# Kernel optimization log

Hardware: AMD Instinct MI355X
Metric: run time of the kernel (lower is better)

## Reference

```python
import jax, jax.numpy as jnp
import numpy as np

B, H, W, C = 4, 64, 64, 256
D = C // 8  # reduction_ratio = 8


def setup_inputs() -> dict:
    key = jax.random.key(0)
    ks = jax.random.split(key, 6)
    scale = 1.0 / np.sqrt(C)
    return {
        "x": jax.random.normal(ks[0], (B, H, W, C), dtype=jnp.float32),
        "Wf": jax.random.normal(ks[1], (C, D), dtype=jnp.float32) * scale,
        "Wg": jax.random.normal(ks[2], (C, D), dtype=jnp.float32) * scale,
        "Wh": jax.random.normal(ks[3], (C, D), dtype=jnp.float32) * scale,
        "Wv": jax.random.normal(ks[4], (D, C), dtype=jnp.float32) * (1.0 / np.sqrt(D)),
        "gamma": jax.random.normal(ks[5], (), dtype=jnp.float32),
    }


def reference(x, Wf, Wg, Wh, Wv, gamma):
    b, h, w, c = x.shape
    n = h * w
    xf = x.reshape(b, n, c)
    # 1x1 convs (no bias) == per-pixel matmuls over channels
    q = xf @ Wf  # [b, n, d]
    k = xf @ Wg  # [b, n, d]
    v = xf @ Wh  # [b, n, d]
    # beta[i, j] = k_i . q_j ; softmax over last (query) axis, unscaled
    beta = jax.nn.softmax(jnp.einsum('bnd,bmd->bnm', k, q), axis=-1)  # [b, n, n]
    o = jnp.einsum('bnm,bmd->bnd', beta, v)  # [b, n, d]
    o = o.reshape(b, h, w, -1) @ Wv  # output 1x1 conv -> [b, h, w, c]
    return gamma * o + x
```

## Files before the change

### kernel.cpp

```cpp
#include <hip/hip_runtime.h>
#include <hip/hip_bf16.h>
#include <stdint.h>


typedef __attribute__((ext_vector_type(8))) short bf16x8;
typedef __attribute__((ext_vector_type(4))) short bf16x4;
typedef __attribute__((ext_vector_type(4))) float f32x4;
typedef unsigned short ushort_t;

static __device__ __forceinline__ ushort_t f2bf(float f) {
    __hip_bfloat16 h = __float2bfloat16(f);
    return __builtin_bit_cast(ushort_t, h);
}
static __device__ __forceinline__ float bf2f(ushort_t u) {
    return __bfloat162float(__builtin_bit_cast(__hip_bfloat16, u));
}

static __device__ __forceinline__ f32x4 mfma16bf(bf16x4 a, bf16x4 b, f32x4 c) {
#if __has_builtin(__builtin_amdgcn_mfma_f32_16x16x16bf16_1k)
    return __builtin_amdgcn_mfma_f32_16x16x16bf16_1k(a, b, c, 0, 0, 0);
#else
    f32x4 d;
    asm("v_mfma_f32_16x16x16_bf16 %0, %1, %2, %3"
        : "=v"(d) : "v"(a), "v"(b), "v"(c));
    return d;
#endif
}

#define NROWS 16384
#define NTOK  4096
#define QKS   40
#define OPART (NROWS * 32)

__global__ __launch_bounds__(256) void qkv_kernel(
    const float* __restrict__ x,
    const float* __restrict__ Wf, const float* __restrict__ Wg,
    const float* __restrict__ Wh,
    ushort_t* __restrict__ qh,
    ushort_t* __restrict__ kh, ushort_t* __restrict__ kl,
    ushort_t* __restrict__ vT)
{
    __shared__ __align__(16) ushort_t xh[32 * QKS];
    __shared__ __align__(16) ushort_t xl[32 * QKS];

    const int tid  = threadIdx.x;
    const int wave = tid >> 6;
    const int lane = tid & 63;
    const int ln15 = lane & 15;
    const int quad = lane >> 4;
    const int row0 = blockIdx.x * 32;
    const int rg     = wave & 1;
    const int cgbase = wave >> 1;
    const int r  = tid >> 3;
    const int pp = (tid & 7) * 4;

    f32x4 acc[3];
    #pragma unroll
    for (int ci = 0; ci < 3; ++ci) acc[ci] = (f32x4){0.f, 0.f, 0.f, 0.f};

    float4 xa = *reinterpret_cast<const float4*>(&x[(row0 + r) * 256 + pp]);

    for (int k0 = 0; k0 < 256; k0 += 32) {
        bf16x8 bh[3], bl[3];
        #pragma unroll
        for (int ci = 0; ci < 3; ++ci) {
            int cg = cgbase + ci * 2;
            const float* Wsrc = (cg < 2) ? Wf : (cg < 4) ? Wg : Wh;
            int c = (cg & 1) * 16 + ln15;
            ushort_t hv8[8], lv8[8];
            #pragma unroll
            for (int j = 0; j < 8; ++j) {
                float w = Wsrc[(k0 + quad * 8 + j) * 32 + c];
                ushort_t hi = f2bf(w);
                hv8[j] = hi;
                lv8[j] = f2bf(w - bf2f(hi));
            }
            bh[ci] = *reinterpret_cast<bf16x8*>(hv8);
            bl[ci] = *reinterpret_cast<bf16x8*>(lv8);
        }
        float fv[4];
        *reinterpret_cast<float4*>(fv) = xa;
        ushort_t hv[4], lv[4];
        #pragma unroll
        for (int j = 0; j < 4; ++j) {
            hv[j] = f2bf(fv[j]);
            lv[j] = f2bf(fv[j] - bf2f(hv[j]));
        }
        __syncthreads();
        *reinterpret_cast<uint2*>(&xh[r * QKS + pp]) = *reinterpret_cast<uint2*>(hv);
        *reinterpret_cast<uint2*>(&xl[r * QKS + pp]) = *reinterpret_cast<uint2*>(lv);
        __syncthreads();
        if (k0 < 224)
            xa = *reinterpret_cast<const float4*>(&x[(row0 + r) * 256 + k0 + 32 + pp]);

        const bf16x8 ah = *reinterpret_cast<const bf16x8*>(
            &xh[(rg * 16 + ln15) * QKS + quad * 8]);
        const bf16x8 al = *reinterpret_cast<const bf16x8*>(
            &xl[(rg * 16 + ln15) * QKS + quad * 8]);
        #pragma unroll
        for (int ci = 0; ci < 3; ++ci) {
            acc[ci] = __builtin_amdgcn_mfma_f32_16x16x32_bf16(ah, bh[ci], acc[ci], 0, 0, 0);
            acc[ci] = __builtin_amdgcn_mfma_f32_16x16x32_bf16(al, bh[ci], acc[ci], 0, 0, 0);
            acc[ci] = __builtin_amdgcn_mfma_f32_16x16x32_bf16(ah, bl[ci], acc[ci], 0, 0, 0);
        }
    }

    #pragma unroll
    for (int ci = 0; ci < 3; ++ci) {
        int cg = cgbase + ci * 2;
        int cc = (cg & 1) * 16 + ln15;
        int rowb = row0 + rg * 16 + quad * 4;
        if (cg < 2) {
            #pragma unroll
            for (int rr = 0; rr < 4; ++rr)
                qh[(rowb + rr) * 32 + cc] = f2bf(acc[ci][rr]);
        } else if (cg < 4) {
            #pragma unroll
            for (int rr = 0; rr < 4; ++rr) {
                float val = acc[ci][rr];
                ushort_t hi = f2bf(val);
                kh[(rowb + rr) * 32 + cc] = hi;
                kl[(rowb + rr) * 32 + cc] = f2bf(val - bf2f(hi));
            }
        } else {
            int bb = row0 >> 12;
            int m  = (row0 & 4095) + rg * 16 + quad * 4;
            ushort4 h4;
            h4.x = f2bf(acc[ci][0]);
            h4.y = f2bf(acc[ci][1]);
            h4.z = f2bf(acc[ci][2]);
            h4.w = f2bf(acc[ci][3]);
            *reinterpret_cast<ushort4*>(&vT[bb * 131072 + cc * 4096 + m]) = h4;
        }
    }
}

__global__ __launch_bounds__(256, 4) void attn_kernel(
    const ushort_t* __restrict__ qhg,
    const ushort_t* __restrict__ khg, const ushort_t* __restrict__ klg,
    const ushort_t* __restrict__ vT,
    float* __restrict__ o_part, float* __restrict__ l_part)
{
    __shared__ float Ored[4][32][65];
    __shared__ float Lred[4][64];

    const int tid  = threadIdx.x;
    const int wave = tid >> 6;
    const int lane = tid & 63;
    const int ln15 = lane & 15;
    const int quad = lane >> 4;

    const int rowtile = blockIdx.x & 255;
    const int chunk   = blockIdx.x >> 8;
    const int b    = rowtile >> 6;
    const int n0   = (rowtile & 63) * 64;
    const int base = b * NTOK;
    const int bb   = b * 131072;

    bf16x8 khf[4], klf[4];
    #pragma unroll
    for (int t = 0; t < 4; ++t) {
        khf[t] = *reinterpret_cast<const bf16x8*>(
            &khg[(base + n0 + t * 16 + ln15) * 32 + quad * 8]);
        klf[t] = *reinterpret_cast<const bf16x8*>(
            &klg[(base + n0 + t * 16 + ln15) * 32 + quad * 8]);
    }

    f32x4 accO[2][4];
    #pragma unroll
    for (int s01 = 0; s01 < 2; ++s01)
        #pragma unroll
        for (int t = 0; t < 4; ++t)
            accO[s01][t] = (f32x4){0.f, 0.f, 0.f, 0.f};
    float lacc[4] = {0.f, 0.f, 0.f, 0.f};

    const int mbase = chunk * 1024 + wave * 16;
    const ushort_t* qp  = qhg + (size_t)(base + mbase + ln15) * 32 + quad * 8;
    const ushort_t* vp0 = vT + bb + ln15 * 4096 + mbase + quad * 4;
    const ushort_t* vp1 = vp0 + 16 * 4096;

    for (int it = 0; it < 16; ++it) {
        const bf16x8 qf  = *reinterpret_cast<const bf16x8*>(qp);
        const bf16x4 va0 = *reinterpret_cast<const bf16x4*>(vp0);
        const bf16x4 va1 = *reinterpret_cast<const bf16x4*>(vp1);
        qp  += 64 * 32;
        vp0 += 64;
        vp1 += 64;

        #pragma unroll
        for (int t = 0; t < 4; ++t) {
            f32x4 s = __builtin_amdgcn_mfma_f32_16x16x32_bf16(
                qf, khf[t], (f32x4){0.f, 0.f, 0.f, 0.f}, 0, 0, 0);
            s = __builtin_amdgcn_mfma_f32_16x16x32_bf16(qf, klf[t], s, 0, 0, 0);

            float p0 = __expf(s[0]);
            float p1 = __expf(s[1]);
            float p2 = __expf(s[2]);
            float p3 = __expf(s[3]);
            lacc[t] += (p0 + p1) + (p2 + p3);

            ushort_t pu[4];
            pu[0] = f2bf(p0);
            pu[1] = f2bf(p1);
            pu[2] = f2bf(p2);
            pu[3] = f2bf(p3);
            const bf16x4 pb = *reinterpret_cast<bf16x4*>(pu);

            accO[0][t] = mfma16bf(va0, pb, accO[0][t]);
            accO[1][t] = mfma16bf(va1, pb, accO[1][t]);
        }
    }

    #pragma unroll
    for (int s01 = 0; s01 < 2; ++s01)
        #pragma unroll
        for (int t = 0; t < 4; ++t)
            #pragma unroll
            for (int rr = 0; rr < 4; ++rr)
                Ored[wave][s01 * 16 + quad * 4 + rr][t * 16 + ln15] = accO[s01][t][rr];

    #pragma unroll
    for (int t = 0; t < 4; ++t) {
        float v = lacc[t];
        v += __shfl_xor(v, 16);
        v += __shfl_xor(v, 32);
        if (quad == 0) Lred[wave][t * 16 + ln15] = v;
    }
    __syncthreads();

    const int rowb = base + n0;
    float* op = o_part + (size_t)chunk * OPART;
    #pragma unroll
    for (int e = 0; e < 8; ++e) {
        int idx = e * 256 + tid;
        int d = idx & 31;
        int n = idx >> 5;
        float v = Ored[0][d][n] + Ored[1][d][n] + Ored[2][d][n] + Ored[3][d][n];
        op[(rowb + n) * 32 + d] = v;
    }
    if (tid < 64) {
        l_part[chunk * NROWS + rowb + tid] =
            Lred[0][tid] + Lred[1][tid] + Lred[2][tid] + Lred[3][tid];
    }
}

__global__ __launch_bounds__(256) void out_kernel(
    const float* __restrict__ o_part, const float* __restrict__ l_part,
    const float* __restrict__ Wv, const float* __restrict__ x,
    const float* __restrict__ gamma, float* __restrict__ out)
{
    __shared__ float wv[8192];
    __shared__ float orow[32][32];
    __shared__ float linv[32];
    const int tid  = threadIdx.x;
    const int row0 = blockIdx.x * 32;

    for (int i = tid; i < 8192; i += 256) wv[i] = Wv[i];
    for (int i = tid; i < 1024; i += 256) {
        int rr = i >> 5, d = i & 31;
        int idx = (row0 + rr) * 32 + d;
        orow[rr][d] = o_part[idx] + o_part[OPART + idx]
                    + o_part[2 * OPART + idx] + o_part[3 * OPART + idx];
    }
    if (tid < 32) {
        int row = row0 + tid;
        linv[tid] = 1.0f / (l_part[row] + l_part[NROWS + row]
                          + l_part[2 * NROWS + row] + l_part[3 * NROWS + row]);
    }
    __syncthreads();

    const float g = gamma[0];
    #pragma unroll 4
    for (int rc = 0; rc < 32; rc += 8) {
        float acc[8];
        #pragma unroll
        for (int rr = 0; rr < 8; ++rr) acc[rr] = 0.f;
        for (int d = 0; d < 32; ++d) {
            float wvd = wv[d * 256 + tid];
            #pragma unroll
            for (int rr = 0; rr < 8; ++rr) acc[rr] += orow[rc + rr][d] * wvd;
        }
        #pragma unroll
        for (int rr = 0; rr < 8; ++rr) {
            int row = row0 + rc + rr;
            out[row * 256 + tid] = g * acc[rr] * linv[rc + rr] + x[row * 256 + tid];
        }
    }
}

extern "C" void kernel_launch(void* const* d_in, const int* in_sizes, int n_in,
                              void* d_out, int out_size, void* d_ws, size_t ws_size,
                              hipStream_t stream)
{
    const float* x     = (const float*)d_in[0];
    const float* Wf    = (const float*)d_in[1];
    const float* Wg    = (const float*)d_in[2];
    const float* Wh    = (const float*)d_in[3];
    const float* Wv    = (const float*)d_in[4];
    const float* gamma = (const float*)d_in[5];
    float* out = (float*)d_out;

    ushort_t* qh = (ushort_t*)d_ws;
    ushort_t* kh = qh + NROWS * 32;
    ushort_t* kl = kh + NROWS * 32;
    ushort_t* vT = kl + NROWS * 32;
    float* o_part = (float*)(vT + NROWS * 32);
    float* l_part = o_part + (size_t)4 * OPART;

    qkv_kernel<<<dim3(512), dim3(256), 0, stream>>>(x, Wf, Wg, Wh, qh, kh, kl, vT);
    attn_kernel<<<dim3(1024), dim3(256), 0, stream>>>(qh, kh, kl, vT, o_part, l_part);
    out_kernel<<<dim3(512), dim3(256), 0, stream>>>(o_part, l_part, Wv, x, gamma, out);
}
```

Measured before the change: 122.7 us.

## Fuse output projection into attention kernel and use exp2 with prescaled queries

The separate output kernel is removed. Each attention block now spans all 4096 keys with 8 waves, reduces O and the row sums in shared memory, and applies the Wv projection, gamma scale and residual add directly. This drops the split-chunk partial buffers, their global round trip and one kernel launch. Queries are pre-multiplied by log2(e) so the hardware exp2 can replace __expf. In exchange the grid shrinks to 256 blocks of 512 threads, which may underfill the GPU and lower occupancy, and shared memory use per block grows.

```diff
diff --git a/kernel.cpp b/kernel.cpp
--- a/kernel.cpp
+++ b/kernel.cpp
@@ -27,10 +27,18 @@
 #endif
 }
 
+static __device__ __forceinline__ float fexp2(float x) {
+#if __has_builtin(__builtin_amdgcn_exp2f)
+    return __builtin_amdgcn_exp2f(x);
+#else
+    return exp2f(x);
+#endif
+}
+
 #define NROWS 16384
 #define NTOK  4096
 #define QKS   40
-#define OPART (NROWS * 32)
+#define LOG2E 1.44269504088896340736f
 
 __global__ __launch_bounds__(256) void qkv_kernel(
     const float* __restrict__ x,
@@ -113,7 +121,7 @@
         if (cg < 2) {
             #pragma unroll
             for (int rr = 0; rr < 4; ++rr)
-                qh[(rowb + rr) * 32 + cc] = f2bf(acc[ci][rr]);
+                qh[(rowb + rr) * 32 + cc] = f2bf(acc[ci][rr] * LOG2E);
         } else if (cg < 4) {
             #pragma unroll
             for (int rr = 0; rr < 4; ++rr) {
@@ -135,14 +143,18 @@
     }
 }
 
-__global__ __launch_bounds__(256, 4) void attn_kernel(
+__global__ __launch_bounds__(512, 2) void attn_kernel(
     const ushort_t* __restrict__ qhg,
     const ushort_t* __restrict__ khg, const ushort_t* __restrict__ klg,
     const ushort_t* __restrict__ vT,
-    float* __restrict__ o_part, float* __restrict__ l_part)
+    const float* __restrict__ Wv, const float* __restrict__ x,
+    const float* __restrict__ gamma, float* __restrict__ out)
 {
-    __shared__ float Ored[4][32][65];
-    __shared__ float Lred[4][64];
+    __shared__ float Ored[8][32][65];
+    __shared__ float Lred[8][64];
+    __shared__ float wv[8192];
+    __shared__ float Os[64][33];
+    __shared__ float linv[64];
 
     const int tid  = threadIdx.x;
     const int wave = tid >> 6;
@@ -150,10 +162,8 @@
     const int ln15 = lane & 15;
     const int quad = lane >> 4;
 
-    const int rowtile = blockIdx.x & 255;
-    const int chunk   = blockIdx.x >> 8;
-    const int b    = rowtile >> 6;
-    const int n0   = (rowtile & 63) * 64;
+    const int b    = blockIdx.x >> 6;
+    const int n0   = (blockIdx.x & 63) * 64;
     const int base = b * NTOK;
     const int bb   = b * 131072;
 
@@ -166,6 +176,9 @@
             &klg[(base + n0 + t * 16 + ln15) * 32 + quad * 8]);
     }
 
+    #pragma unroll
+    for (int i = 0; i < 16; ++i) wv[tid + i * 512] = Wv[tid + i * 512];
+
     f32x4 accO[2][4];
     #pragma unroll
     for (int s01 = 0; s01 < 2; ++s01)
@@ -174,18 +187,18 @@
             accO[s01][t] = (f32x4){0.f, 0.f, 0.f, 0.f};
     float lacc[4] = {0.f, 0.f, 0.f, 0.f};
 
-    const int mbase = chunk * 1024 + wave * 16;
+    const int mbase = wave * 16;
     const ushort_t* qp  = qhg + (size_t)(base + mbase + ln15) * 32 + quad * 8;
     const ushort_t* vp0 = vT + bb + ln15 * 4096 + mbase + quad * 4;
     const ushort_t* vp1 = vp0 + 16 * 4096;
 
-    for (int it = 0; it < 16; ++it) {
+    for (int it = 0; it < 32; ++it) {
         const bf16x8 qf  = *reinterpret_cast<const bf16x8*>(qp);
         const bf16x4 va0 = *reinterpret_cast<const bf16x4*>(vp0);
         const bf16x4 va1 = *reinterpret_cast<const bf16x4*>(vp1);
-        qp  += 64 * 32;
-        vp0 += 64;
-        vp1 += 64;
+        qp  += 128 * 32;
+        vp0 += 128;
+        vp1 += 128;
 
         #pragma unroll
         for (int t = 0; t < 4; ++t) {
@@ -193,10 +206,10 @@
                 qf, khf[t], (f32x4){0.f, 0.f, 0.f, 0.f}, 0, 0, 0);
             s = __builtin_amdgcn_mfma_f32_16x16x32_bf16(qf, klf[t], s, 0, 0, 0);
 
-            float p0 = __expf(s[0]);
-            float p1 = __expf(s[1]);
-            float p2 = __expf(s[2]);
-            float p3 = __expf(s[3]);
+            float p0 = fexp2(s[0]);
+            float p1 = fexp2(s[1]);
+            float p2 = fexp2(s[2]);
+            float p3 = fexp2(s[3]);
             lacc[t] += (p0 + p1) + (p2 + p3);
 
             ushort_t pu[4];
@@ -228,62 +241,40 @@
     }
     __syncthreads();
 
-    const int rowb = base + n0;
-    float* op = o_part + (size_t)chunk * OPART;
-    #pragma unroll
-    for (int e = 0; e < 8; ++e) {
-        int idx = e * 256 + tid;
+    #pragma unroll
+    for (int i = 0; i < 4; ++i) {
+        int idx = i * 512 + tid;
         int d = idx & 31;
         int n = idx >> 5;
-        float v = Ored[0][d][n] + Ored[1][d][n] + Ored[2][d][n] + Ored[3][d][n];
-        op[(rowb + n) * 32 + d] = v;
+        float v = (Ored[0][d][n] + Ored[1][d][n]) + (Ored[2][d][n] + Ored[3][d][n])
+                + (Ored[4][d][n] + Ored[5][d][n]) + (Ored[6][d][n] + Ored[7][d][n]);
+        Os[n][d] = v;
     }
     if (tid < 64) {
-        l_part[chunk * NROWS + rowb + tid] =
-            Lred[0][tid] + Lred[1][tid] + Lred[2][tid] + Lred[3][tid];
-    }
-}
-
-__global__ __launch_bounds__(256) void out_kernel(
-    const float* __restrict__ o_part, const float* __restrict__ l_part,
-    const float* __restrict__ Wv, const float* __restrict__ x,
-    const float* __restrict__ gamma, float* __restrict__ out)
-{
-    __shared__ float wv[8192];
-    __shared__ float orow[32][32];
-    __shared__ float linv[32];
-    const int tid  = threadIdx.x;
-    const int row0 = blockIdx.x * 32;
-
-    for (int i = tid; i < 8192; i += 256) wv[i] = Wv[i];
-    for (int i = tid; i < 1024; i += 256) {
-        int rr = i >> 5, d = i & 31;
-        int idx = (row0 + rr) * 32 + d;
-        orow[rr][d] = o_part[idx] + o_part[OPART + idx]
-                    + o_part[2 * OPART + idx] + o_part[3 * OPART + idx];
-    }
-    if (tid < 32) {
-        int row = row0 + tid;
-        linv[tid] = 1.0f / (l_part[row] + l_part[NROWS + row]
-                          + l_part[2 * NROWS + row] + l_part[3 * NROWS + row]);
+        float s = (Lred[0][tid] + Lred[1][tid]) + (Lred[2][tid] + Lred[3][tid])
+                + (Lred[4][tid] + Lred[5][tid]) + (Lred[6][tid] + Lred[7][tid]);
+        linv[tid] = 1.0f / s;
     }
     __syncthreads();
 
-    const float g = gamma[0];
-    #pragma unroll 4
+    const float g  = gamma[0];
+    const int   c  = tid & 255;
+    const int   nh = (tid >> 8) * 32;
+    const int rowb = base + n0 + nh;
+    #pragma unroll
     for (int rc = 0; rc < 32; rc += 8) {
         float acc[8];
         #pragma unroll
         for (int rr = 0; rr < 8; ++rr) acc[rr] = 0.f;
         for (int d = 0; d < 32; ++d) {
-            float wvd = wv[d * 256 + tid];
-            #pragma unroll
-            for (int rr = 0; rr < 8; ++rr) acc[rr] += orow[rc + rr][d] * wvd;
+            float wvd = wv[d * 256 + c];
+            #pragma unroll
+            for (int rr = 0; rr < 8; ++rr) acc[rr] += Os[nh + rc + rr][d] * wvd;
         }
         #pragma unroll
         for (int rr = 0; rr < 8; ++rr) {
-            int row = row0 + rc + rr;
-            out[row * 256 + tid] = g * acc[rr] * linv[rc + rr] + x[row * 256 + tid];
+            int row = rowb + rc + rr;
+            out[row * 256 + c] = g * acc[rr] * linv[nh + rc + rr] + x[row * 256 + c];
         }
     }
 }
@@ -304,10 +295,7 @@
     ushort_t* kh = qh + NROWS * 32;
     ushort_t* kl = kh + NROWS * 32;
     ushort_t* vT = kl + NROWS * 32;
-    float* o_part = (float*)(vT + NROWS * 32);
-    float* l_part = o_part + (size_t)4 * OPART;
 
     qkv_kernel<<<dim3(512), dim3(256), 0, stream>>>(x, Wf, Wg, Wh, qh, kh, kl, vT);
-    attn_kernel<<<dim3(1024), dim3(256), 0, stream>>>(qh, kh, kl, vT, o_part, l_part);
-    out_kernel<<<dim3(512), dim3(256), 0, stream>>>(o_part, l_part, Wv, x, gamma, out);
-}
+    attn_kernel<<<dim3(256), dim3(512), 0, stream>>>(qh, kh, kl, vT, Wv, x, gamma, out);
+}
```

After: 113.4 us. 1.08x faster.
